# Kernel optimization log

Hardware: AMD Instinct MI355X
Metric: run time of the kernel (lower is better)

Reference implementation:

```python
import jax, jax.numpy as jnp
import numpy as np

N = 50000        # num nodes
E = 800000       # num edges (avg degree 16)
IN_DIM = 64
OUT_DIM = 64
PE_DIM = 24
HEADS = 2
HID = OUT_DIM * HEADS  # 128


def setup_inputs() -> dict:
    key = jax.random.key(0)
    ks = jax.random.split(key, 16)
    std = 0.1  # trunc_normal_(std=0.1) init in the torch module
    return {
        "x": jax.random.normal(ks[0], (N, IN_DIM), jnp.float32),
        "pe_index": jax.random.randint(ks[1], (2, E), 0, N, jnp.int32),
        "pe_val": jax.random.normal(ks[2], (E, PE_DIM), jnp.float32),
        # edge-weight MLP (blocks): input proj, one residual FFN block, final proj
        "W_in": jax.random.normal(ks[3], (PE_DIM, HID), jnp.float32) * std,
        "b_in": jnp.zeros((HID,), jnp.float32),
        "W1": jax.random.normal(ks[4], (HID, HID), jnp.float32) * std,
        "b1": jnp.zeros((HID,), jnp.float32),
        "W2": jax.random.normal(ks[5], (HID, HID), jnp.float32) * std,
        "b2": jnp.zeros((HID,), jnp.float32),
        "W_fin": jax.random.normal(ks[6], (HID, HID), jnp.float32) * std,
        "b_fin": jnp.zeros((HID,), jnp.float32),
        # node feature -> multi-head projection
        "W_x": jax.random.normal(ks[7], (IN_DIM, HID), jnp.float32) * std,
        "b_x": jnp.zeros((HID,), jnp.float32),
        # per-head output bias
        "head_bias": jnp.zeros((1, HEADS, OUT_DIM), jnp.float32),
        # final out projection
        "W_out": jax.random.normal(ks[8], (HID, OUT_DIM), jnp.float32) * std,
        "b_out": jnp.zeros((OUT_DIM,), jnp.float32),
    }


def _edge_mlp(pe, W_in, b_in, W1, b1, W2, b2, W_fin, b_fin):
    # Linear(pe_dim->hid), then residual block [GELU, Linear, GELU, Linear, +res], then Linear(hid->hid)
    g = lambda t: jax.nn.gelu(t, approximate=False)  # torch nn.GELU default = exact erf
    x0 = pe @ W_in + b_in                     # [E, HID]
    h = g(x0) @ W1 + b1
    h = g(h) @ W2 + b2
    x0 = h + x0                               # ResidualLayer: x + x_res
    return x0 @ W_fin + b_fin                 # [E, HID]


def reference(x, pe_index, pe_val, W_in, b_in, W1, b1, W2, b2, W_fin, b_fin,
              W_x, b_x, head_bias, W_out, b_out):
    tgt = pe_index[0]  # messages aggregate to edge_index[0]
    src = pe_index[1]
    score = _edge_mlp(pe_val, W_in, b_in, W1, b1, W2, b2, W_fin, b_fin)
    score = score.reshape(-1, HEADS, OUT_DIM)                 # [E, H, D]
    xh = (x @ W_x + b_x).reshape(-1, HEADS, OUT_DIM)          # [N, H, D]
    msg = xh[src] * score                                     # gather-multiply
    wV = jax.ops.segment_sum(msg, tgt, num_segments=N)        # scatter-add [N, H, D]
    deg = jax.ops.segment_sum(jnp.ones((msg.shape[0],), jnp.float32), tgt, num_segments=N)
    wV = wV / jnp.maximum(deg, 1.0)[:, None, None]            # average=True -> mean aggregation
    h = (wV + head_bias).reshape(-1, HEADS * OUT_DIM)
    return h @ W_out + b_out                                  # out_proj: [N, OUT_DIM]
```

## Files before the change

### kernel.cpp

```cpp
#include <hip/hip_runtime.h>
#include <hip/hip_bf16.h>
#include <math.h>

#define NN 50000
#define EE 800000
#define HID 128
#define PED 24
#define IND 64
#define OUTD 64
#define EBLK 128
#define AKS 136

typedef short bf16x8 __attribute__((ext_vector_type(8)));
typedef float f32x4 __attribute__((ext_vector_type(4)));

__device__ __forceinline__ float gelu_fast(float x) {
    float x2 = x * x;
    float t = __builtin_fmaf(x2, -0.07135481627f, -1.5957691216f);
    float e = __expf(x * t);
    return x * __builtin_amdgcn_rcpf(1.0f + e);
}
__device__ __forceinline__ unsigned short f2bf(float f) {
    unsigned int u = __float_as_uint(f);
    u = (u + 0x7fffu + ((u >> 16) & 1u)) >> 16;
    return (unsigned short)u;
}
__device__ __forceinline__ unsigned int pkbf2(float a, float b) {
    __hip_bfloat162 h = __float22bfloat162_rn(make_float2(a, b));
    return *reinterpret_cast<unsigned int*>(&h);
}
__device__ __forceinline__ float bflo(unsigned int u) {
    return __uint_as_float(u << 16);
}
__device__ __forceinline__ float bfhi(unsigned int u) {
    return __uint_as_float(u & 0xffff0000u);
}

__global__ __launch_bounds__(256) void pre_kernel(
    const float* __restrict__ x, const float* __restrict__ W_x,
    const float* __restrict__ b_x, unsigned short* __restrict__ xhb,
    const float* __restrict__ W_in, const float* __restrict__ W1,
    const float* __restrict__ W2, const float* __restrict__ Wf,
    unsigned short* __restrict__ WT_in, unsigned short* __restrict__ WT1,
    unsigned short* __restrict__ WT2, unsigned short* __restrict__ WTf,
    float* __restrict__ wV, int* __restrict__ cnt) {
    int bx = blockIdx.x;
    if (bx < 6250) {
        int gid = bx * 256 + threadIdx.x;
        int n = gid >> 5;
        int q = gid & 31;
        *(float4*)&wV[(size_t)n * HID + q * 4] = make_float4(0.f, 0.f, 0.f, 0.f);
        const float4* xr4 = (const float4*)(x + (size_t)n * IND);
        float4 acc = *(const float4*)&b_x[q * 4];
#pragma unroll 4
        for (int k4 = 0; k4 < 16; k4++) {
            float4 xv = xr4[k4];
            {
                float xk = xv.x;
                float4 w = *(const float4*)&W_x[(k4 * 4 + 0) * HID + q * 4];
                acc.x += xk * w.x; acc.y += xk * w.y;
                acc.z += xk * w.z; acc.w += xk * w.w;
            }
            {
                float xk = xv.y;
                float4 w = *(const float4*)&W_x[(k4 * 4 + 1) * HID + q * 4];
                acc.x += xk * w.x; acc.y += xk * w.y;
                acc.z += xk * w.z; acc.w += xk * w.w;
            }
            {
                float xk = xv.z;
                float4 w = *(const float4*)&W_x[(k4 * 4 + 2) * HID + q * 4];
                acc.x += xk * w.x; acc.y += xk * w.y;
                acc.z += xk * w.z; acc.w += xk * w.w;
            }
            {
                float xk = xv.w;
                float4 w = *(const float4*)&W_x[(k4 * 4 + 3) * HID + q * 4];
                acc.x += xk * w.x; acc.y += xk * w.y;
                acc.z += xk * w.z; acc.w += xk * w.w;
            }
        }
        uint2 p;
        p.x = pkbf2(acc.x, acc.y);
        p.y = pkbf2(acc.z, acc.w);
        ((uint2*)&xhb[(size_t)n * HID])[q] = p;
    } else {
        int idx = (bx - 6250) * 256 + threadIdx.x;
        if (idx < NN) cnt[idx] = 0;
        if (idx < 4096) {
            int j = idx >> 5, k = idx & 31;
            WT_in[idx] = f2bf(k < PED ? W_in[k * HID + j] : 0.f);
        } else if (idx < 4096 + 16384) {
            int i = idx - 4096; int j = i >> 7, k = i & 127;
            WT1[i] = f2bf(W1[k * HID + j]);
        } else if (idx < 4096 + 32768) {
            int i = idx - 4096 - 16384; int j = i >> 7, k = i & 127;
            WT2[i] = f2bf(W2[k * HID + j]);
        } else if (idx < 4096 + 49152) {
            int i = idx - 4096 - 32768; int j = i >> 7, k = i & 127;
            WTf[i] = f2bf(Wf[k * HID + j]);
        }
    }
}

__global__ __launch_bounds__(256) void hist_kernel(const int* __restrict__ pe_idx,
                                                   int* __restrict__ cnt) {
    int e4 = blockIdx.x * 256 + threadIdx.x;
    if (e4 < EE / 4) {
        int4 t = *(const int4*)&pe_idx[e4 * 4];
        atomicAdd(&cnt[t.x], 1);
        atomicAdd(&cnt[t.y], 1);
        atomicAdd(&cnt[t.z], 1);
        atomicAdd(&cnt[t.w], 1);
    }
}

__global__ __launch_bounds__(1024) void scan_kernel(const int* __restrict__ cnt,
                                                    int* __restrict__ woff) {
    __shared__ int s_w[16];
    int tid = threadIdx.x;
    const int chunk = 52;
    int base = tid * chunk;
    int end = base + chunk; if (end > NN) end = NN;
    int s = 0;
    if (base + chunk <= NN) {
#pragma unroll
        for (int i = 0; i < 13; i++) {
            int4 v4 = *(const int4*)&cnt[base + i * 4];
            s += v4.x + v4.y + v4.z + v4.w;
        }
    } else {
        for (int i = base; i < end; i++) s += cnt[i];
    }
    int v = s;
    int lane = tid & 63, wid = tid >> 6;
#pragma unroll
    for (int d = 1; d < 64; d <<= 1) {
        int u = __shfl_up(v, d, 64);
        if (lane >= d) v += u;
    }
    if (lane == 63) s_w[wid] = v;
    __syncthreads();
    if (tid < 16) {
        int wv = s_w[tid];
#pragma unroll
        for (int d = 1; d < 16; d <<= 1) {
            int u = __shfl_up(wv, d, 64);
            if (tid >= d) wv += u;
        }
        s_w[tid] = wv;
    }
    __syncthreads();
    int exc = v - s + (wid ? s_w[wid - 1] : 0);
    int run = exc;
    for (int i = base; i < end; i++) { woff[i] = run; run += cnt[i]; }
}

__global__ __launch_bounds__(256) void scatter_kernel(const int* __restrict__ pe_idx,
                                                      int* __restrict__ woff,
                                                      int* __restrict__ perm) {
    int e4 = blockIdx.x * 256 + threadIdx.x;
    if (e4 < EE / 4) {
        int4 t = *(const int4*)&pe_idx[e4 * 4];
        int e = e4 * 4;
        perm[atomicAdd(&woff[t.x], 1)] = e + 0;
        perm[atomicAdd(&woff[t.y], 1)] = e + 1;
        perm[atomicAdd(&woff[t.z], 1)] = e + 2;
        perm[atomicAdd(&woff[t.w], 1)] = e + 3;
    }
}

__global__ __launch_bounds__(512, 4) void edge_kernel(
    const float* __restrict__ pe_val, const int* __restrict__ pe_idx,
    const int* __restrict__ perm, const unsigned short* __restrict__ xhb,
    const unsigned short* __restrict__ WT_in, const unsigned short* __restrict__ WT1,
    const unsigned short* __restrict__ WT2, const unsigned short* __restrict__ WTf,
    const float* __restrict__ b_in, const float* __restrict__ b1,
    const float* __restrict__ b2, const float* __restrict__ bfin,
    float* __restrict__ wV) {
    __shared__ __align__(16) unsigned short s_act[EBLK][AKS];
    __shared__ __align__(16) unsigned short s_W[HID][AKS];
    __shared__ __align__(16) unsigned short s_pe[EBLK][32];
    __shared__ int s_tgt[EBLK], s_src[EBLK];

    const int tid = threadIdx.x;
    const int lane = tid & 63;
    const int w = tid >> 6;
    const int cg = w & 3;
    const int eh = w >> 2;
    const int ebase = eh * 64;
    const int l15 = lane & 15;
    const int quad = lane >> 4;
    const long b0 = (long)blockIdx.x * EBLK;

    if (tid < EBLK) {
        int eid = perm[b0 + tid];
        s_tgt[tid] = pe_idx[eid];
        s_src[tid] = pe_idx[EE + eid];
    }
#pragma unroll
    for (int i = 0; i < 4; i++) {
        int idx = tid + i * 512; int r = idx >> 4, seg = idx & 15;
        *(uint4*)&s_W[r][seg * 8] = *(const uint4*)&WT1[r * HID + seg * 8];
    }
#pragma unroll
    for (int i = 0; i < 4; i++) {
        int idx = tid + i * 512; int e = idx >> 4, k2 = idx & 15;
        float2 v = make_float2(0.f, 0.f);
        if (k2 < 12) {
            int eid = perm[b0 + e];
            v = *(const float2*)&pe_val[(size_t)eid * PED + k2 * 2];
        }
        *(unsigned int*)&s_pe[e][k2 * 2] = pkbf2(v.x, v.y);
    }
    __syncthreads();

    f32x4 C[2][4];
    uint2 x0pk[2][4];

    {
        float4 ba = *(const float4*)&b_in[(2 * cg + 0) * 16 + quad * 4];
        float4 bb = *(const float4*)&b_in[(2 * cg + 1) * 16 + quad * 4];
        f32x4 ci0 = {ba.x, ba.y, ba.z, ba.w};
        f32x4 ci1 = {bb.x, bb.y, bb.z, bb.w};
        bf16x8 a0 = *(const bf16x8*)&WT_in[((2 * cg + 0) * 16 + l15) * 32 + quad * 8];
        bf16x8 a1 = *(const bf16x8*)&WT_in[((2 * cg + 1) * 16 + l15) * 32 + quad * 8];
        __builtin_amdgcn_s_setprio(1);
#pragma unroll
        for (int u = 0; u < 4; u++) {
            bf16x8 bfr = *(const bf16x8*)&s_pe[ebase + u * 16 + l15][quad * 8];
            C[0][u] = __builtin_amdgcn_mfma_f32_16x16x32_bf16(a0, bfr, ci0, 0, 0, 0);
            C[1][u] = __builtin_amdgcn_mfma_f32_16x16x32_bf16(a1, bfr, ci1, 0, 0, 0);
        }
        __builtin_amdgcn_s_setprio(0);
    }
#pragma unroll
    for (int t = 0; t < 2; t++) {
        int ch0 = (2 * cg + t) * 16 + quad * 4;
#pragma unroll
        for (int u = 0; u < 4; u++) {
            int e = ebase + u * 16 + l15;
            f32x4 c = C[t][u];
            x0pk[t][u].x = pkbf2(c[0], c[1]);
            x0pk[t][u].y = pkbf2(c[2], c[3]);
            uint2 p;
            p.x = pkbf2(gelu_fast(c[0]), gelu_fast(c[1]));
            p.y = pkbf2(gelu_fast(c[2]), gelu_fast(c[3]));
            *(uint2*)&s_act[e][ch0] = p;
        }
    }
    __syncthreads();

#define GEMM128(BIAS)                                                          \
    {                                                                          \
        float4 ba_ = *(const float4*)&(BIAS)[(2 * cg + 0) * 16 + quad * 4];    \
        float4 bb_ = *(const float4*)&(BIAS)[(2 * cg + 1) * 16 + quad * 4];    \
        f32x4 ci0 = {ba_.x, ba_.y, ba_.z, ba_.w};                              \
        f32x4 ci1 = {bb_.x, bb_.y, bb_.z, bb_.w};                              \
        _Pragma("unroll") for (int u = 0; u < 4; u++) {                        \
            C[0][u] = ci0; C[1][u] = ci1;                                      \
        }                                                                      \
        __builtin_amdgcn_s_setprio(1);                                         \
        _Pragma("unroll") for (int ks = 0; ks < 4; ks++) {                     \
            bf16x8 a0 = *(const bf16x8*)&s_W[(2 * cg + 0) * 16 + l15]          \
                                            [ks * 32 + quad * 8];              \
            bf16x8 a1 = *(const bf16x8*)&s_W[(2 * cg + 1) * 16 + l15]          \
                                            [ks * 32 + quad * 8];              \
            _Pragma("unroll") for (int u = 0; u < 4; u++) {                    \
                bf16x8 bfr = *(const bf16x8*)&s_act[ebase + u * 16 + l15]      \
                                                   [ks * 32 + quad * 8];       \
                C[0][u] = __builtin_amdgcn_mfma_f32_16x16x32_bf16(a0, bfr,     \
                                                                  C[0][u], 0, 0, 0); \
                C[1][u] = __builtin_amdgcn_mfma_f32_16x16x32_bf16(a1, bfr,     \
                                                                  C[1][u], 0, 0, 0); \
            }                                                                  \
        }                                                                      \
        __builtin_amdgcn_s_setprio(0);                                         \
    }

#define STAGE_W(WT)                                                            \
    _Pragma("unroll") for (int i = 0; i < 4; i++) {                            \
        int idx = tid + i * 512; int r = idx >> 4, seg = idx & 15;             \
        *(uint4*)&s_W[r][seg * 8] = *(const uint4*)&(WT)[r * HID + seg * 8];   \
    }

    GEMM128(b1);
    __syncthreads();
#pragma unroll
    for (int t = 0; t < 2; t++) {
        int ch0 = (2 * cg + t) * 16 + quad * 4;
#pragma unroll
        for (int u = 0; u < 4; u++) {
            int e = ebase + u * 16 + l15;
            f32x4 c = C[t][u];
            uint2 p;
            p.x = pkbf2(gelu_fast(c[0]), gelu_fast(c[1]));
            p.y = pkbf2(gelu_fast(c[2]), gelu_fast(c[3]));
            *(uint2*)&s_act[e][ch0] = p;
        }
    }
    STAGE_W(WT2);
    __syncthreads();

    GEMM128(b2);
    __syncthreads();
#pragma unroll
    for (int t = 0; t < 2; t++) {
        int ch0 = (2 * cg + t) * 16 + quad * 4;
#pragma unroll
        for (int u = 0; u < 4; u++) {
            int e = ebase + u * 16 + l15;
            f32x4 c = C[t][u];
            uint2 p;
            p.x = pkbf2(c[0] + bflo(x0pk[t][u].x), c[1] + bfhi(x0pk[t][u].x));
            p.y = pkbf2(c[2] + bflo(x0pk[t][u].y), c[3] + bfhi(x0pk[t][u].y));
            *(uint2*)&s_act[e][ch0] = p;
        }
    }
    STAGE_W(WTf);
    __syncthreads();

    GEMM128(bfin);
    const int e0 = w * 16;
    unsigned int xv[16];
#pragma unroll
    for (int j = 0; j < 16; j++) {
        xv[j] = *(const unsigned int*)&xhb[(size_t)s_src[e0 + j] * HID + lane * 2];
    }
    __syncthreads();
#pragma unroll
    for (int t = 0; t < 2; t++) {
        int ch0 = (2 * cg + t) * 16 + quad * 4;
#pragma unroll
        for (int u = 0; u < 4; u++) {
            int e = ebase + u * 16 + l15;
            f32x4 c = C[t][u];
            uint2 p;
            p.x = pkbf2(c[0], c[1]);
            p.y = pkbf2(c[2], c[3]);
            *(uint2*)&s_act[e][ch0] = p;
        }
    }
    __syncthreads();

    {
        float a0 = 0.f, a1 = 0.f;
        int prev = s_tgt[e0];
        bool firstseg = true;
#pragma unroll
        for (int j = 0; j < 16; j++) {
            int tg = s_tgt[e0 + j];
            if (tg != prev) {
                float* wp = &wV[(size_t)prev * HID + lane * 2];
                if (firstseg) { atomicAdd(wp, a0); atomicAdd(wp + 1, a1); }
                else          { *(float2*)wp = make_float2(a0, a1); }
                firstseg = false;
                a0 = a1 = 0.f;
                prev = tg;
            }
            unsigned int sv = *(const unsigned int*)&s_act[e0 + j][lane * 2];
            unsigned int xu = xv[j];
            a0 += bflo(xu) * bflo(sv);
            a1 += bfhi(xu) * bfhi(sv);
        }
        float* wp = &wV[(size_t)prev * HID + lane * 2];
        atomicAdd(wp, a0); atomicAdd(wp + 1, a1);
    }
#undef GEMM128
#undef STAGE_W
}

__global__ __launch_bounds__(256) void out_kernel(
    const float* __restrict__ wV, const int* __restrict__ cnt,
    const float* __restrict__ head_bias, const float* __restrict__ W_out,
    const float* __restrict__ b_out, float* __restrict__ out) {
    int gid = blockIdx.x * 256 + threadIdx.x;
    int n = gid >> 4;
    int q = gid & 15;
    if (n >= NN) return;
    float inv = 1.0f / fmaxf((float)cnt[n], 1.0f);
    const float4* wr4p = (const float4*)(wV + (size_t)n * HID);
    const float4* hb4p = (const float4*)head_bias;
    float4 acc = *(const float4*)&b_out[q * 4];
#pragma unroll 2
    for (int k4 = 0; k4 < 32; k4++) {
        float4 wr4 = wr4p[k4];
        float4 hb4 = hb4p[k4];
        {
            float hv = __builtin_fmaf(wr4.x, inv, hb4.x);
            float4 w4 = *(const float4*)&W_out[(k4 * 4 + 0) * OUTD + q * 4];
            acc.x += hv * w4.x; acc.y += hv * w4.y;
            acc.z += hv * w4.z; acc.w += hv * w4.w;
        }
        {
            float hv = __builtin_fmaf(wr4.y, inv, hb4.y);
            float4 w4 = *(const float4*)&W_out[(k4 * 4 + 1) * OUTD + q * 4];
            acc.x += hv * w4.x; acc.y += hv * w4.y;
            acc.z += hv * w4.z; acc.w += hv * w4.w;
        }
        {
            float hv = __builtin_fmaf(wr4.z, inv, hb4.z);
            float4 w4 = *(const float4*)&W_out[(k4 * 4 + 2) * OUTD + q * 4];
            acc.x += hv * w4.x; acc.y += hv * w4.y;
            acc.z += hv * w4.z; acc.w += hv * w4.w;
        }
        {
            float hv = __builtin_fmaf(wr4.w, inv, hb4.w);
            float4 w4 = *(const float4*)&W_out[(k4 * 4 + 3) * OUTD + q * 4];
            acc.x += hv * w4.x; acc.y += hv * w4.y;
            acc.z += hv * w4.z; acc.w += hv * w4.w;
        }
    }
    *(float4*)&out[(size_t)n * OUTD + q * 4] = acc;
}

extern "C" void kernel_launch(void* const* d_in, const int* in_sizes, int n_in,
                              void* d_out, int out_size, void* d_ws, size_t ws_size,
                              hipStream_t stream) {
    const float* x      = (const float*)d_in[0];
    const int*   pe_idx = (const int*)d_in[1];
    const float* pe_val = (const float*)d_in[2];
    const float* W_in   = (const float*)d_in[3];
    const float* b_in   = (const float*)d_in[4];
    const float* W1     = (const float*)d_in[5];
    const float* b1     = (const float*)d_in[6];
    const float* W2     = (const float*)d_in[7];
    const float* b2     = (const float*)d_in[8];
    const float* Wf     = (const float*)d_in[9];
    const float* bfin   = (const float*)d_in[10];
    const float* W_x    = (const float*)d_in[11];
    const float* b_x    = (const float*)d_in[12];
    const float* hb     = (const float*)d_in[13];
    const float* W_out  = (const float*)d_in[14];
    const float* b_out  = (const float*)d_in[15];
    float* out = (float*)d_out;

    float* wV   = (float*)d_ws;
    int*   cnt  = (int*)(wV + (size_t)NN * HID);
    int*   woff = cnt + NN;
    int*   perm = woff + NN;
    unsigned short* WT_in = (unsigned short*)(perm + EE);
    unsigned short* WT1   = WT_in + 128 * 32;
    unsigned short* WT2   = WT1 + 128 * 128;
    unsigned short* WTf   = WT2 + 128 * 128;
    unsigned short* xhb   = WTf + 128 * 128;

    pre_kernel<<<6250 + 208, 256, 0, stream>>>(x, W_x, b_x, xhb,
                                               W_in, W1, W2, Wf,
                                               WT_in, WT1, WT2, WTf, wV, cnt);
    hist_kernel<<<(EE / 4 + 255) / 256, 256, 0, stream>>>(pe_idx, cnt);
    scan_kernel<<<1, 1024, 0, stream>>>(cnt, woff);
    scatter_kernel<<<(EE / 4 + 255) / 256, 256, 0, stream>>>(pe_idx, woff, perm);

    edge_kernel<<<EE / EBLK, 512, 0, stream>>>(pe_val, pe_idx, perm, xhb,
                                               WT_in, WT1, WT2, WTf,
                                               b_in, b1, b2, bfin, wV);

    out_kernel<<<(NN * 16 + 255) / 256, 256, 0, stream>>>(wV, cnt, hb, W_out,
                                                          b_out, out);
}
```

Baseline: 587.1 us.

## Stage edge-MLP weights via async global-to-LDS loads with XOR swizzle

Weight matrices are pre-swizzled with an XOR pattern on the host-side prep kernel so they can be copied straight into unpadded LDS with global_load_lds, issued right after the previous GEMM so the copy overlaps the activation epilogue. The MFMA A-fragment reads apply the same swizzle to avoid bank conflicts. The histogram and scatter kernels also switch from four edges per thread to one edge per thread. Correctness depends on the async LDS writes being complete before the barrier, since no explicit vmcnt wait is added.

```diff
diff --git a/kernel.cpp b/kernel.cpp
--- a/kernel.cpp
+++ b/kernel.cpp
@@ -35,6 +35,11 @@
 __device__ __forceinline__ float bfhi(unsigned int u) {
     return __uint_as_float(u & 0xffff0000u);
 }
+
+#define GLL16(GP, LP)                                                          \
+    __builtin_amdgcn_global_load_lds(                                          \
+        (const __attribute__((address_space(1))) unsigned int*)(GP),           \
+        (__attribute__((address_space(3))) unsigned int*)(LP), 16, 0, 0)
 
 __global__ __launch_bounds__(256) void pre_kernel(
     const float* __restrict__ x, const float* __restrict__ W_x,
@@ -91,28 +96,22 @@
             int j = idx >> 5, k = idx & 31;
             WT_in[idx] = f2bf(k < PED ? W_in[k * HID + j] : 0.f);
         } else if (idx < 4096 + 16384) {
-            int i = idx - 4096; int j = i >> 7, k = i & 127;
-            WT1[i] = f2bf(W1[k * HID + j]);
+            int i = idx - 4096; int r = i >> 7, k = i & 127;
+            WT1[r * 128 + (k ^ ((r & 7) << 3))] = f2bf(W1[k * HID + r]);
         } else if (idx < 4096 + 32768) {
-            int i = idx - 4096 - 16384; int j = i >> 7, k = i & 127;
-            WT2[i] = f2bf(W2[k * HID + j]);
+            int i = idx - 4096 - 16384; int r = i >> 7, k = i & 127;
+            WT2[r * 128 + (k ^ ((r & 7) << 3))] = f2bf(W2[k * HID + r]);
         } else if (idx < 4096 + 49152) {
-            int i = idx - 4096 - 32768; int j = i >> 7, k = i & 127;
-            WTf[i] = f2bf(Wf[k * HID + j]);
+            int i = idx - 4096 - 32768; int r = i >> 7, k = i & 127;
+            WTf[r * 128 + (k ^ ((r & 7) << 3))] = f2bf(Wf[k * HID + r]);
         }
     }
 }
 
 __global__ __launch_bounds__(256) void hist_kernel(const int* __restrict__ pe_idx,
                                                    int* __restrict__ cnt) {
-    int e4 = blockIdx.x * 256 + threadIdx.x;
-    if (e4 < EE / 4) {
-        int4 t = *(const int4*)&pe_idx[e4 * 4];
-        atomicAdd(&cnt[t.x], 1);
-        atomicAdd(&cnt[t.y], 1);
-        atomicAdd(&cnt[t.z], 1);
-        atomicAdd(&cnt[t.w], 1);
-    }
+    int e = blockIdx.x * 256 + threadIdx.x;
+    if (e < EE) atomicAdd(&cnt[pe_idx[e]], 1);
 }
 
 __global__ __launch_bounds__(1024) void scan_kernel(const int* __restrict__ cnt,
@@ -159,14 +158,11 @@
 __global__ __launch_bounds__(256) void scatter_kernel(const int* __restrict__ pe_idx,
                                                       int* __restrict__ woff,
                                                       int* __restrict__ perm) {
-    int e4 = blockIdx.x * 256 + threadIdx.x;
-    if (e4 < EE / 4) {
-        int4 t = *(const int4*)&pe_idx[e4 * 4];
-        int e = e4 * 4;
-        perm[atomicAdd(&woff[t.x], 1)] = e + 0;
-        perm[atomicAdd(&woff[t.y], 1)] = e + 1;
-        perm[atomicAdd(&woff[t.z], 1)] = e + 2;
-        perm[atomicAdd(&woff[t.w], 1)] = e + 3;
+    int e = blockIdx.x * 256 + threadIdx.x;
+    if (e < EE) {
+        int t = pe_idx[e];
+        int p = atomicAdd(&woff[t], 1);
+        perm[p] = e;
     }
 }
 
@@ -179,7 +175,7 @@
     const float* __restrict__ b2, const float* __restrict__ bfin,
     float* __restrict__ wV) {
     __shared__ __align__(16) unsigned short s_act[EBLK][AKS];
-    __shared__ __align__(16) unsigned short s_W[HID][AKS];
+    __shared__ __align__(16) unsigned short s_W[HID * HID];
     __shared__ __align__(16) unsigned short s_pe[EBLK][32];
     __shared__ int s_tgt[EBLK], s_src[EBLK];
 
@@ -191,17 +187,20 @@
     const int ebase = eh * 64;
     const int l15 = lane & 15;
     const int quad = lane >> 4;
+    const int swzE = (l15 & 7) << 3;
     const long b0 = (long)blockIdx.x * EBLK;
+
+#define STAGE_W_ASYNC(WT)                                                      \
+    _Pragma("unroll") for (int i = 0; i < 4; i++) {                            \
+        int c = w * 4 + i;                                                     \
+        GLL16((WT) + c * 512 + lane * 8, s_W + c * 512);                       \
+    }
+    STAGE_W_ASYNC(WT1);
 
     if (tid < EBLK) {
         int eid = perm[b0 + tid];
         s_tgt[tid] = pe_idx[eid];
         s_src[tid] = pe_idx[EE + eid];
-    }
-#pragma unroll
-    for (int i = 0; i < 4; i++) {
-        int idx = tid + i * 512; int r = idx >> 4, seg = idx & 15;
-        *(uint4*)&s_W[r][seg * 8] = *(const uint4*)&WT1[r * HID + seg * 8];
     }
 #pragma unroll
     for (int i = 0; i < 4; i++) {
@@ -262,10 +261,11 @@
         }                                                                      \
         __builtin_amdgcn_s_setprio(1);                                         \
         _Pragma("unroll") for (int ks = 0; ks < 4; ks++) {                     \
-            bf16x8 a0 = *(const bf16x8*)&s_W[(2 * cg + 0) * 16 + l15]          \
-                                            [ks * 32 + quad * 8];              \
-            bf16x8 a1 = *(const bf16x8*)&s_W[(2 * cg + 1) * 16 + l15]          \
-                                            [ks * 32 + quad * 8];              \
+            int wo = (ks * 32 + quad * 8) ^ swzE;                              \
+            bf16x8 a0 = *(const bf16x8*)&s_W[((2 * cg + 0) * 16 + l15) * HID   \
+                                             + wo];                            \
+            bf16x8 a1 = *(const bf16x8*)&s_W[((2 * cg + 1) * 16 + l15) * HID   \
+                                             + wo];                            \
             _Pragma("unroll") for (int u = 0; u < 4; u++) {                    \
                 bf16x8 bfr = *(const bf16x8*)&s_act[ebase + u * 16 + l15]      \
                                                    [ks * 32 + quad * 8];       \
@@ -278,14 +278,9 @@
         __builtin_amdgcn_s_setprio(0);                                         \
     }
 
-#define STAGE_W(WT)                                                            \
-    _Pragma("unroll") for (int i = 0; i < 4; i++) {                            \
-        int idx = tid + i * 512; int r = idx >> 4, seg = idx & 15;             \
-        *(uint4*)&s_W[r][seg * 8] = *(const uint4*)&(WT)[r * HID + seg * 8];   \
-    }
-
     GEMM128(b1);
     __syncthreads();
+    STAGE_W_ASYNC(WT2);
 #pragma unroll
     for (int t = 0; t < 2; t++) {
         int ch0 = (2 * cg + t) * 16 + quad * 4;
@@ -299,11 +294,11 @@
             *(uint2*)&s_act[e][ch0] = p;
         }
     }
-    STAGE_W(WT2);
     __syncthreads();
 
     GEMM128(b2);
     __syncthreads();
+    STAGE_W_ASYNC(WTf);
 #pragma unroll
     for (int t = 0; t < 2; t++) {
         int ch0 = (2 * cg + t) * 16 + quad * 4;
@@ -317,7 +312,6 @@
             *(uint2*)&s_act[e][ch0] = p;
         }
     }
-    STAGE_W(WTf);
     __syncthreads();
 
     GEMM128(bfin);
@@ -367,7 +361,7 @@
         atomicAdd(wp, a0); atomicAdd(wp + 1, a1);
     }
 #undef GEMM128
-#undef STAGE_W
+#undef STAGE_W_ASYNC
 }
 
 __global__ __launch_bounds__(256) void out_kernel(
@@ -448,9 +442,9 @@
     pre_kernel<<<6250 + 208, 256, 0, stream>>>(x, W_x, b_x, xhb,
                                                W_in, W1, W2, Wf,
                                                WT_in, WT1, WT2, WTf, wV, cnt);
-    hist_kernel<<<(EE / 4 + 255) / 256, 256, 0, stream>>>(pe_idx, cnt);
+    hist_kernel<<<(EE + 255) / 256, 256, 0, stream>>>(pe_idx, cnt);
     scan_kernel<<<1, 1024, 0, stream>>>(cnt, woff);
-    scatter_kernel<<<(EE / 4 + 255) / 256, 256, 0, stream>>>(pe_idx, woff, perm);
+    scatter_kernel<<<(EE + 255) / 256, 256, 0, stream>>>(pe_idx, woff, perm);
 
     edge_kernel<<<EE / EBLK, 512, 0, stream>>>(pe_val, pe_idx, perm, xhb,
                                                WT_in, WT1, WT2, WTf,
```

Result: slower. 604.0 us (+2.9%).
